# Kernel tuning notes

Measured on AMD Instinct MI355X. Metric: run time of the kernel, lower is better.

Reference implementation:

```python
import jax, jax.numpy as jnp
import numpy as np

NUM_FREQS = 10  # get_embedder_nerf(10, input_dims=3) -> 3 + 3*2*10 = 63 dims


def nerf_embed(x):
    # x: [..., 3]; order per NeRF embedder: [x, sin(f0*x), cos(f0*x), sin(f1*x), ...]
    freqs = (2.0 ** jnp.arange(NUM_FREQS)).astype(x.dtype)           # [10]
    xb = x[..., None, :] * freqs[:, None]                            # [..., 10, 3]
    sc = jnp.stack([jnp.sin(xb), jnp.cos(xb)], axis=-2)              # [..., 10, 2, 3]
    return jnp.concatenate([x, sc.reshape(x.shape[:-1] + (60,))], axis=-1)


def setup_inputs() -> dict:
    key = jax.random.key(0)
    ks = jax.random.split(key, 16)
    B, H, W = 4, 256, 256
    V, F = 50000, 100000
    FEAT, SHAPE_FEAT, STYLE = 256, 128, 256
    D_IN = FEAT + SHAPE_FEAT + 63 + STYLE  # 703
    HID = 256
    s = 0.05
    return {
        "pix_to_face": jax.random.randint(ks[0], (B, H, W), 0, F),
        "bary_coords": jax.random.uniform(ks[1], (B, H, W, 3), dtype=jnp.float32),
        "faces": jax.random.randint(ks[2], (F, 3), 0, V),
        "feature": jax.random.normal(ks[3], (V, FEAT), dtype=jnp.float32),
        "shape_features": jax.random.normal(ks[4], (V, SHAPE_FEAT), dtype=jnp.float32),
        "color_bg": jax.random.uniform(ks[5], (B, 3, 1, 1), dtype=jnp.float32),
        "style_latent": jax.random.normal(ks[6], (1, STYLE), dtype=jnp.float32),
        "w1": jax.random.normal(ks[7], (D_IN, HID), dtype=jnp.float32) * s,
        "b1": jax.random.normal(ks[8], (HID,), dtype=jnp.float32) * s,
        "w2": jax.random.normal(ks[9], (HID, HID), dtype=jnp.float32) * s,
        "b2": jax.random.normal(ks[10], (HID,), dtype=jnp.float32) * s,
        "w3": jax.random.normal(ks[11], (HID, 3), dtype=jnp.float32) * s,
        "b3": jax.random.normal(ks[12], (3,), dtype=jnp.float32) * s,
    }


def reference(pix_to_face, bary_coords, faces, feature, shape_features,
              color_bg, style_latent, w1, b1, w2, b2, w3, b3):
    B, H, W = pix_to_face.shape
    mask = pix_to_face > 0                                           # foreground pixels
    vidx = faces[pix_to_face]                                        # [B,H,W,3] vertex ids
    # gather per-vertex features then barycentric-weighted mean over the 3 verts
    fv = feature[vidx]                                               # [B,H,W,3,256]
    ff = jnp.einsum('bhwvc,bhwv->bhwc', fv, bary_coords) / 3.0       # .mean(dim=3)
    sv = shape_features[vidx]                                        # [B,H,W,3,128]
    sf = jnp.einsum('bhwvc,bhwv->bhwc', sv, bary_coords) / 3.0
    emb = nerf_embed(bary_coords)                                    # [B,H,W,63]
    style = jnp.broadcast_to(style_latent[0], (B, H, W, style_latent.shape[-1]))
    x = jnp.concatenate([ff, sf, emb, style], axis=-1)               # [B,H,W,703]
    h = jax.nn.relu(x @ w1 + b1)
    h = jax.nn.relu(h @ w2 + b2)
    out = jax.nn.relu(h @ w3 + b3)                                   # mlp ends with ReLU
    colors = out - 1.0                                               # use_act=True, tanh=False
    bg = color_bg[:, :, 0, 0][:, None, None, :]                      # [B,1,1,3]
    buf = jnp.where(mask[..., None], colors, bg)                     # scatter to image
    return jnp.concatenate([buf, mask.astype(buf.dtype)[..., None]], axis=-1)  # [B,H,W,4]
```

## Files before the change

### kernel.cpp

```cpp
#include <hip/hip_runtime.h>
#include <math.h>


typedef _Float16 hv8 __attribute__((ext_vector_type(8)));
typedef __attribute__((ext_vector_type(4))) float f32x4;

#define TILE_M 64

__device__ inline int swzE(int row, int k) { return row * 64  + (k ^ ((row & 7) << 3)); }
__device__ inline int swzH(int row, int k) { return row * 256 + (k ^ ((row & 7) << 3)); }
__device__ inline int swzA(int row, int k) { return row * 384 + (k ^ ((row & 7) << 3)); }

__global__ __launch_bounds__(256)
void prep_weights(const float* __restrict__ style,
                  const float* __restrict__ w1, const float* __restrict__ b1,
                  const float* __restrict__ w2, const float* __restrict__ w3,
                  _Float16* __restrict__ w1T, _Float16* __restrict__ w2T,
                  _Float16* __restrict__ w3T, float* __restrict__ b1p)
{
    const int j = blockIdx.x;
    const int t = threadIdx.x;
    if (j < 256) {
        float part = style[t] * w1[(size_t)(447 + t) * 256 + j];
        #pragma unroll
        for (int off = 32; off; off >>= 1) part += __shfl_down(part, off, 64);
        __shared__ float red[4];
        if ((t & 63) == 0) red[t >> 6] = part;
        __syncthreads();
        if (t == 0) b1p[j] = b1[j] + red[0] + red[1] + red[2] + red[3];
        for (int k = t; k < 448; k += 256) {
            float v = (k < 447) ? w1[(size_t)k * 256 + j] : 0.0f;
            if (k < 384) v *= (1.0f / 3.0f);
            w1T[(size_t)j * 448 + k] = (_Float16)v;
        }
    } else if (j < 512) {
        const int jj = j - 256;
        w2T[(size_t)jj * 256 + t] = (_Float16)w2[(size_t)t * 256 + jj];
    } else {
        #pragma unroll
        for (int r = 0; r < 16; ++r)
            w3T[r * 256 + t] = (r < 3) ? (_Float16)w3[t * 3 + r] : (_Float16)0.0f;
    }
}

__global__ __launch_bounds__(256, 2)
void pgemm(const float* __restrict__ feat, const float* __restrict__ shp,
           const _Float16* __restrict__ w1T, _Float16* __restrict__ P, int nV)
{
    __shared__ _Float16 as[64 * 384];
    const int tid = threadIdx.x;
    const int n0 = blockIdx.x * 64;
    const int lane = tid & 63, wv = tid >> 6;
    const int nbase = wv << 6, l15 = lane & 15, kq = lane >> 4;

    const hv8* bp[4];
    #pragma unroll
    for (int nf = 0; nf < 4; ++nf)
        bp[nf] = (const hv8*)(w1T + (size_t)(nbase + nf * 16 + l15) * 448 + (kq << 3));
    hv8 bv[3][4];
    auto loadB = [&](int t, hv8* dst) {
        #pragma unroll
        for (int nf = 0; nf < 4; ++nf) dst[nf] = bp[nf][t << 2];
    };
    loadB(0, bv[0]); loadB(1, bv[1]); loadB(2, bv[2]);

    #pragma unroll
    for (int i = 0; i < 12; ++i) {
        const int id = tid + i * 256;
        const int row = id / 48;
        const int g = id - row * 48;
        int v = n0 + row; if (v >= nV) v = nV - 1;
        const float* s = (g < 32) ? (feat + (size_t)v * 256 + g * 8)
                                  : (shp  + (size_t)v * 128 + (g - 32) * 8);
        const float4 a = ((const float4*)s)[0];
        const float4 b = ((const float4*)s)[1];
        hv8 h = { (_Float16)a.x, (_Float16)a.y, (_Float16)a.z, (_Float16)a.w,
                  (_Float16)b.x, (_Float16)b.y, (_Float16)b.z, (_Float16)b.w };
        *(hv8*)(&as[swzA(row, g * 8)]) = h;
    }
    f32x4 acc[4][4];
    #pragma unroll
    for (int mf = 0; mf < 4; ++mf)
        #pragma unroll
        for (int nf = 0; nf < 4; ++nf) acc[mf][nf] = (f32x4){0.f, 0.f, 0.f, 0.f};
    __syncthreads();

    auto loadA = [&](int t, hv8* dst) {
        #pragma unroll
        for (int mf = 0; mf < 4; ++mf)
            dst[mf] = *(const hv8*)(as + swzA(mf * 16 + l15, (t << 5) | (kq << 3)));
    };
    hv8 av[2][4];
    loadA(0, av[0]);
    #pragma unroll
    for (int t = 0; t < 12; ++t) {
        if (t + 1 < 12) loadA(t + 1, av[(t + 1) & 1]);
        const hv8* avt = av[t & 1];
        const hv8* bvt = bv[t % 3];
        __builtin_amdgcn_s_setprio(1);
        #pragma unroll
        for (int mf = 0; mf < 4; ++mf)
            #pragma unroll
            for (int nf = 0; nf < 4; ++nf)
                acc[mf][nf] = __builtin_amdgcn_mfma_f32_16x16x32_f16(avt[mf], bvt[nf], acc[mf][nf], 0, 0, 0);
        __builtin_amdgcn_s_setprio(0);
        if (t + 3 < 12) loadB(t + 3, bv[t % 3]);
    }
    #pragma unroll
    for (int mf = 0; mf < 4; ++mf)
        #pragma unroll
        for (int nf = 0; nf < 4; ++nf) {
            const int col = nbase + nf * 16 + l15;
            const int r0 = mf * 16 + (kq << 2);
            #pragma unroll
            for (int r = 0; r < 4; ++r) {
                const int v = n0 + r0 + r;
                if (v < nV) P[(size_t)v * 256 + col] = (_Float16)acc[mf][nf][r];
            }
        }
}

__global__ __launch_bounds__(512, 4)
void renderer(const int* __restrict__ pix, const float* __restrict__ bary,
              const int* __restrict__ faces,
              const _Float16* __restrict__ P,
              const float* __restrict__ color_bg,
              const float* __restrict__ b2g,
              const float* __restrict__ b3,
              const _Float16* __restrict__ w1T,
              const _Float16* __restrict__ w2T,
              const _Float16* __restrict__ w3T,
              const float* __restrict__ b1p,
              float* __restrict__ out)
{
    __shared__ _Float16 embs[64 * 64];
    __shared__ _Float16 pb[64 * 256];
    __shared__ int   vidx[TILE_M][3];
    __shared__ float bcs[TILE_M][3];

    const int tid = threadIdx.x;
    const int cpx = gridDim.x >> 3;
    const int bid = (blockIdx.x & 7) * cpx + (blockIdx.x >> 3);
    const int n0  = bid * TILE_M;

    const int lane  = tid & 63;
    const int wv    = tid >> 6;
    const int nbase = wv << 5;
    const int l15   = lane & 15;
    const int kq    = lane >> 4;

    if (tid < TILE_M) {
        const int n = n0 + tid;
        const int face = pix[n];
        vidx[tid][0] = faces[face * 3 + 0];
        vidx[tid][1] = faces[face * 3 + 1];
        vidx[tid][2] = faces[face * 3 + 2];
        bcs[tid][0] = bary[n * 3 + 0];
        bcs[tid][1] = bary[n * 3 + 1];
        bcs[tid][2] = bary[n * 3 + 2];
    }
    __syncthreads();

    const int gp = tid >> 5;
    const int c8 = (tid & 31) << 3;

    hv8 g0[3], g1[3];
    auto loadG = [&](hv8* g, const int b) {
        const int p = b * 16 + gp;
        g[0] = *(const hv8*)(P + (size_t)vidx[p][0] * 256 + c8);
        g[1] = *(const hv8*)(P + (size_t)vidx[p][1] * 256 + c8);
        g[2] = *(const hv8*)(P + (size_t)vidx[p][2] * 256 + c8);
    };
    auto blendG = [&](hv8* g, const int b) {
        const int p = b * 16 + gp;
        const _Float16 c0 = (_Float16)bcs[p][0];
        const _Float16 c1 = (_Float16)bcs[p][1];
        const _Float16 c2 = (_Float16)bcs[p][2];
        *(hv8*)(&pb[swzH(p, c8)]) = g[0] * c0 + g[1] * c1 + g[2] * c2;
    };

    loadG(g0, 0);
    loadG(g1, 1);

    {
        const int p = tid >> 3;
        const int e8 = (tid & 7) << 3;
        const float c0 = bcs[p][0], c1 = bcs[p][1], c2 = bcs[p][2];
        hv8 h;
        #pragma unroll
        for (int i = 0; i < 8; ++i) {
            const int s = e8 + i;
            float v;
            if (s < 3) v = (s == 0) ? c0 : ((s == 1) ? c1 : c2);
            else if (s < 63) {
                const int q = s - 3;
                const int f = q / 6;
                const int rem = q - f * 6;
                const int d = (rem >= 3) ? rem - 3 : rem;
                const float bd = (d == 0) ? c0 : ((d == 1) ? c1 : c2);
                const float arg = bd * (float)(1 << f);
                v = (rem < 3) ? __sinf(arg) : __cosf(arg);
            } else v = 0.0f;
            h[i] = (_Float16)v;
        }
        *(hv8*)(&embs[swzE(p, e8)]) = h;
    }

    blendG(g0, 0); loadG(g0, 2);
    blendG(g1, 1); loadG(g1, 3);
    blendG(g0, 2);
    blendG(g1, 3);

    f32x4 acc[4][2];
    #pragma unroll
    for (int nf = 0; nf < 2; ++nf) {
        const float b = b1p[nbase + nf * 16 + l15];
        #pragma unroll
        for (int mf = 0; mf < 4; ++mf) acc[mf][nf] = (f32x4){b, b, b, b};
    }
    __syncthreads();

    #pragma unroll
    for (int t = 0; t < 2; ++t) {
        hv8 ave[4], bve[2];
        #pragma unroll
        for (int nf = 0; nf < 2; ++nf)
            bve[nf] = *(const hv8*)(w1T + (size_t)(nbase + nf * 16 + l15) * 448 + 384 + (t << 5) + (kq << 3));
        #pragma unroll
        for (int mf = 0; mf < 4; ++mf)
            ave[mf] = *(const hv8*)(embs + swzE(mf * 16 + l15, (t << 5) | (kq << 3)));
        __builtin_amdgcn_s_setprio(1);
        #pragma unroll
        for (int mf = 0; mf < 4; ++mf)
            #pragma unroll
            for (int nf = 0; nf < 2; ++nf)
                acc[mf][nf] = __builtin_amdgcn_mfma_f32_16x16x32_f16(ave[mf], bve[nf], acc[mf][nf], 0, 0, 0);
        __builtin_amdgcn_s_setprio(0);
    }

    #pragma unroll
    for (int mf = 0; mf < 4; ++mf)
        #pragma unroll
        for (int nf = 0; nf < 2; ++nf) {
            const int col = nbase + nf * 16 + l15;
            const int r0 = mf * 16 + (kq << 2);
            #pragma unroll
            for (int r = 0; r < 4; ++r) {
                const int sl = swzH(r0 + r, col);
                const float pv = (float)pb[sl];
                pb[sl] = (_Float16)fmaxf(acc[mf][nf][r] + pv, 0.0f);
            }
            const float b = b2g[col];
            acc[mf][nf] = (f32x4){b, b, b, b};
        }
    __syncthreads();

    const hv8* bp2[2];
    #pragma unroll
    for (int nf = 0; nf < 2; ++nf)
        bp2[nf] = (const hv8*)(w2T + (size_t)(nbase + nf * 16 + l15) * 256 + (kq << 3));
    #pragma unroll
    for (int t = 0; t < 8; ++t) {
        hv8 av[4], bv[2];
        #pragma unroll
        for (int nf = 0; nf < 2; ++nf) bv[nf] = bp2[nf][t << 2];
        #pragma unroll
        for (int mf = 0; mf < 4; ++mf)
            av[mf] = *(const hv8*)(pb + swzH(mf * 16 + l15, (t << 5) | (kq << 3)));
        __builtin_amdgcn_s_setprio(1);
        #pragma unroll
        for (int mf = 0; mf < 4; ++mf)
            #pragma unroll
            for (int nf = 0; nf < 2; ++nf)
                acc[mf][nf] = __builtin_amdgcn_mfma_f32_16x16x32_f16(av[mf], bv[nf], acc[mf][nf], 0, 0, 0);
        __builtin_amdgcn_s_setprio(0);
    }

    __syncthreads();
    #pragma unroll
    for (int mf = 0; mf < 4; ++mf)
        #pragma unroll
        for (int nf = 0; nf < 2; ++nf) {
            const int col = nbase + nf * 16 + l15;
            const int r0 = mf * 16 + (kq << 2);
            #pragma unroll
            for (int r = 0; r < 4; ++r)
                pb[swzH(r0 + r, col)] = (_Float16)fmaxf(acc[mf][nf][r], 0.0f);
        }

    hv8 bw3[8];
    if (wv < 4) {
        #pragma unroll
        for (int t = 0; t < 8; ++t)
            bw3[t] = *(const hv8*)(w3T + l15 * 256 + ((t << 5) | (kq << 3)));
    }
    __syncthreads();

    if (wv < 4) {
        f32x4 acc3 = (f32x4){0.f, 0.f, 0.f, 0.f};
        #pragma unroll
        for (int t = 0; t < 8; ++t) {
            const hv8 av3 = *(const hv8*)(pb + swzH((wv << 4) + l15, (t << 5) | (kq << 3)));
            acc3 = __builtin_amdgcn_mfma_f32_16x16x32_f16(av3, bw3[t], acc3, 0, 0, 0);
        }
        if (l15 < 4) {
            const int ch = l15;
            #pragma unroll
            for (int r = 0; r < 4; ++r) {
                const int p = (wv << 4) + (kq << 2) + r;
                const int n = n0 + p;
                const bool m = pix[n] > 0;
                float v;
                if (ch == 3) v = m ? 1.0f : 0.0f;
                else         v = m ? (fmaxf(acc3[r] + b3[ch], 0.0f) - 1.0f)
                                   : color_bg[(n >> 16) * 3 + ch];
                out[(size_t)n * 4 + ch] = v;
            }
        }
    }
}

extern "C" void kernel_launch(void* const* d_in, const int* in_sizes, int n_in,
                              void* d_out, int out_size, void* d_ws, size_t ws_size,
                              hipStream_t stream) {
    const int*   pix      = (const int*)  d_in[0];
    const float* bary     = (const float*)d_in[1];
    const int*   faces    = (const int*)  d_in[2];
    const float* feature  = (const float*)d_in[3];
    const float* shapef   = (const float*)d_in[4];
    const float* color_bg = (const float*)d_in[5];
    const float* style    = (const float*)d_in[6];
    const float* w1       = (const float*)d_in[7];
    const float* b1       = (const float*)d_in[8];
    const float* w2       = (const float*)d_in[9];
    const float* b2       = (const float*)d_in[10];
    const float* w3       = (const float*)d_in[11];
    const float* b3       = (const float*)d_in[12];
    float* out = (float*)d_out;

    const int nV = in_sizes[3] / 256;

    char* ws = (char*)d_ws;
    _Float16* w1T  = (_Float16*)ws;
    _Float16* w2T  = (_Float16*)(ws + 229376);
    float*    b1p  = (float*)   (ws + 360448);
    _Float16* w3T  = (_Float16*)(ws + 361472);
    _Float16* Ptab = (_Float16*)(ws + 369664);

    hipLaunchKernelGGL(prep_weights, dim3(513), dim3(256), 0, stream,
                       style, w1, b1, w2, w3, w1T, w2T, w3T, b1p);
    hipLaunchKernelGGL(pgemm, dim3((nV + 63) / 64), dim3(256), 0, stream,
                       feature, shapef, w1T, Ptab, nV);

    const int npix = in_sizes[0];
    hipLaunchKernelGGL(renderer, dim3(npix / TILE_M), dim3(512), 0, stream,
                       pix, bary, faces, Ptab, color_bg,
                       b2, b3, w1T, w2T, w3T, b1p, out);
}
```

Baseline: 183.3 us.

## Process two pixel tiles per block, overlapping next tile's gathers with layer-2 MFMAs

The renderer block now handles 128 pixels as two 64-pixel sub-tiles with double-buffered shared activation tiles and metadata. The vertex-feature gathers, barycentric blend and embedding computation for the second sub-tile are interleaved with the layer-2 MFMA loop of the first, hiding gather latency behind matrix work. The cost is doubled shared memory (about 74KB per block), which may reduce occupancy, and the grid is halved.

```diff
diff --git a/kernel.cpp b/kernel.cpp
--- a/kernel.cpp
+++ b/kernel.cpp
@@ -4,8 +4,6 @@
 
 typedef _Float16 hv8 __attribute__((ext_vector_type(8)));
 typedef __attribute__((ext_vector_type(4))) float f32x4;
-
-#define TILE_M 64
 
 __device__ inline int swzE(int row, int k) { return row * 64  + (k ^ ((row & 7) << 3)); }
 __device__ inline int swzH(int row, int k) { return row * 256 + (k ^ ((row & 7) << 3)); }
@@ -126,74 +124,69 @@
               const _Float16* __restrict__ P,
               const float* __restrict__ color_bg,
               const float* __restrict__ b2g,
-              const float* __restrict__ b3,
+              const float* __restrict__ b3g,
               const _Float16* __restrict__ w1T,
               const _Float16* __restrict__ w2T,
               const _Float16* __restrict__ w3T,
               const float* __restrict__ b1p,
               float* __restrict__ out)
 {
+    __shared__ _Float16 pb[2][64 * 256];
     __shared__ _Float16 embs[64 * 64];
-    __shared__ _Float16 pb[64 * 256];
-    __shared__ int   vidx[TILE_M][3];
-    __shared__ float bcs[TILE_M][3];
+    __shared__ int   vidx[2][64][3];
+    __shared__ float bcs[2][64][3];
 
     const int tid = threadIdx.x;
     const int cpx = gridDim.x >> 3;
     const int bid = (blockIdx.x & 7) * cpx + (blockIdx.x >> 3);
-    const int n0  = bid * TILE_M;
+    const int nb  = bid * 128;
 
     const int lane  = tid & 63;
     const int wv    = tid >> 6;
     const int nbase = wv << 5;
     const int l15   = lane & 15;
     const int kq    = lane >> 4;
-
-    if (tid < TILE_M) {
-        const int n = n0 + tid;
-        const int face = pix[n];
-        vidx[tid][0] = faces[face * 3 + 0];
-        vidx[tid][1] = faces[face * 3 + 1];
-        vidx[tid][2] = faces[face * 3 + 2];
-        bcs[tid][0] = bary[n * 3 + 0];
-        bcs[tid][1] = bary[n * 3 + 1];
-        bcs[tid][2] = bary[n * 3 + 2];
-    }
-    __syncthreads();
-
-    const int gp = tid >> 5;
-    const int c8 = (tid & 31) << 3;
-
+    const int gp    = tid >> 5;
+    const int c8    = (tid & 31) << 3;
+
+    auto metaLoad = [&](int s) {
+        if (tid < 64) {
+            const int n = nb + (s << 6) + tid;
+            const int face = pix[n];
+            vidx[s][tid][0] = faces[face * 3 + 0];
+            vidx[s][tid][1] = faces[face * 3 + 1];
+            vidx[s][tid][2] = faces[face * 3 + 2];
+            bcs[s][tid][0] = bary[n * 3 + 0];
+            bcs[s][tid][1] = bary[n * 3 + 1];
+            bcs[s][tid][2] = bary[n * 3 + 2];
+        }
+    };
     hv8 g0[3], g1[3];
-    auto loadG = [&](hv8* g, const int b) {
-        const int p = b * 16 + gp;
-        g[0] = *(const hv8*)(P + (size_t)vidx[p][0] * 256 + c8);
-        g[1] = *(const hv8*)(P + (size_t)vidx[p][1] * 256 + c8);
-        g[2] = *(const hv8*)(P + (size_t)vidx[p][2] * 256 + c8);
-    };
-    auto blendG = [&](hv8* g, const int b) {
-        const int p = b * 16 + gp;
-        const _Float16 c0 = (_Float16)bcs[p][0];
-        const _Float16 c1 = (_Float16)bcs[p][1];
-        const _Float16 c2 = (_Float16)bcs[p][2];
-        *(hv8*)(&pb[swzH(p, c8)]) = g[0] * c0 + g[1] * c1 + g[2] * c2;
-    };
-
-    loadG(g0, 0);
-    loadG(g1, 1);
-
-    {
+    auto loadG = [&](hv8* g, int s, int b) {
+        const int p = (b << 4) + gp;
+        g[0] = *(const hv8*)(P + (size_t)vidx[s][p][0] * 256 + c8);
+        g[1] = *(const hv8*)(P + (size_t)vidx[s][p][1] * 256 + c8);
+        g[2] = *(const hv8*)(P + (size_t)vidx[s][p][2] * 256 + c8);
+    };
+    auto blendG = [&](hv8* g, int s, int b) {
+        const int p = (b << 4) + gp;
+        const _Float16 d0 = (_Float16)bcs[s][p][0];
+        const _Float16 d1 = (_Float16)bcs[s][p][1];
+        const _Float16 d2 = (_Float16)bcs[s][p][2];
+        *(hv8*)(&pb[s][swzH(p, c8)]) = g[0] * d0 + g[1] * d1 + g[2] * d2;
+    };
+    auto embPhase = [&](int s) {
         const int p = tid >> 3;
         const int e8 = (tid & 7) << 3;
-        const float c0 = bcs[p][0], c1 = bcs[p][1], c2 = bcs[p][2];
+        const float c0 = bcs[s][p][0], c1 = bcs[s][p][1], c2 = bcs[s][p][2];
         hv8 h;
         #pragma unroll
         for (int i = 0; i < 8; ++i) {
-            const int s = e8 + i;
+            const int sl = e8 + i;
             float v;
-            if (s < 3) v = (s == 0) ? c0 : ((s == 1) ? c1 : c2);
-            else if (s < 63) {
-                const int q = s - 3;
+            if (sl < 3) v = (sl == 0) ? c0 : ((sl == 1) ? c1 : c2);
+            else if (sl < 63) {
+                const int q = sl - 3;
                 const int f = q / 6;
                 const int rem = q - f * 6;
                 const int d = (rem >= 3) ? rem - 3 : rem;
@@ -204,69 +197,64 @@
             h[i] = (_Float16)v;
         }
         *(hv8*)(&embs[swzE(p, e8)]) = h;
-    }
-
-    blendG(g0, 0); loadG(g0, 2);
-    blendG(g1, 1); loadG(g1, 3);
-    blendG(g0, 2);
-    blendG(g1, 3);
+    };
 
     f32x4 acc[4][2];
-    #pragma unroll
-    for (int nf = 0; nf < 2; ++nf) {
-        const float b = b1p[nbase + nf * 16 + l15];
-        #pragma unroll
-        for (int mf = 0; mf < 4; ++mf) acc[mf][nf] = (f32x4){b, b, b, b};
-    }
-    __syncthreads();
-
-    #pragma unroll
-    for (int t = 0; t < 2; ++t) {
-        hv8 ave[4], bve[2];
-        #pragma unroll
-        for (int nf = 0; nf < 2; ++nf)
-            bve[nf] = *(const hv8*)(w1T + (size_t)(nbase + nf * 16 + l15) * 448 + 384 + (t << 5) + (kq << 3));
-        #pragma unroll
-        for (int mf = 0; mf < 4; ++mf)
-            ave[mf] = *(const hv8*)(embs + swzE(mf * 16 + l15, (t << 5) | (kq << 3)));
-        __builtin_amdgcn_s_setprio(1);
-        #pragma unroll
-        for (int mf = 0; mf < 4; ++mf)
+    auto accB1 = [&]() {
+        #pragma unroll
+        for (int nf = 0; nf < 2; ++nf) {
+            const float b = b1p[nbase + nf * 16 + l15];
+            #pragma unroll
+            for (int mf = 0; mf < 4; ++mf) acc[mf][nf] = (f32x4){b, b, b, b};
+        }
+    };
+    auto l1mfma = [&]() {
+        #pragma unroll
+        for (int t = 0; t < 2; ++t) {
+            hv8 ave[4], bve[2];
             #pragma unroll
             for (int nf = 0; nf < 2; ++nf)
-                acc[mf][nf] = __builtin_amdgcn_mfma_f32_16x16x32_f16(ave[mf], bve[nf], acc[mf][nf], 0, 0, 0);
-        __builtin_amdgcn_s_setprio(0);
-    }
-
-    #pragma unroll
-    for (int mf = 0; mf < 4; ++mf)
-        #pragma unroll
-        for (int nf = 0; nf < 2; ++nf) {
-            const int col = nbase + nf * 16 + l15;
-            const int r0 = mf * 16 + (kq << 2);
-            #pragma unroll
-            for (int r = 0; r < 4; ++r) {
-                const int sl = swzH(r0 + r, col);
-                const float pv = (float)pb[sl];
-                pb[sl] = (_Float16)fmaxf(acc[mf][nf][r] + pv, 0.0f);
-            }
-            const float b = b2g[col];
-            acc[mf][nf] = (f32x4){b, b, b, b};
-        }
-    __syncthreads();
-
+                bve[nf] = *(const hv8*)(w1T + (size_t)(nbase + nf * 16 + l15) * 448 + 384 + (t << 5) + (kq << 3));
+            #pragma unroll
+            for (int mf = 0; mf < 4; ++mf)
+                ave[mf] = *(const hv8*)(embs + swzE(mf * 16 + l15, (t << 5) | (kq << 3)));
+            __builtin_amdgcn_s_setprio(1);
+            #pragma unroll
+            for (int mf = 0; mf < 4; ++mf)
+                #pragma unroll
+                for (int nf = 0; nf < 2; ++nf)
+                    acc[mf][nf] = __builtin_amdgcn_mfma_f32_16x16x32_f16(ave[mf], bve[nf], acc[mf][nf], 0, 0, 0);
+            __builtin_amdgcn_s_setprio(0);
+        }
+    };
+    auto l1epi = [&](int s) {
+        #pragma unroll
+        for (int mf = 0; mf < 4; ++mf)
+            #pragma unroll
+            for (int nf = 0; nf < 2; ++nf) {
+                const int col = nbase + nf * 16 + l15;
+                const int r0 = mf * 16 + (kq << 2);
+                #pragma unroll
+                for (int r = 0; r < 4; ++r) {
+                    const int sl = swzH(r0 + r, col);
+                    const float pv = (float)pb[s][sl];
+                    pb[s][sl] = (_Float16)fmaxf(acc[mf][nf][r] + pv, 0.0f);
+                }
+                const float b = b2g[col];
+                acc[mf][nf] = (f32x4){b, b, b, b};
+            }
+    };
     const hv8* bp2[2];
     #pragma unroll
     for (int nf = 0; nf < 2; ++nf)
         bp2[nf] = (const hv8*)(w2T + (size_t)(nbase + nf * 16 + l15) * 256 + (kq << 3));
-    #pragma unroll
-    for (int t = 0; t < 8; ++t) {
+    auto l2tile = [&](int s, int t) {
         hv8 av[4], bv[2];
         #pragma unroll
         for (int nf = 0; nf < 2; ++nf) bv[nf] = bp2[nf][t << 2];
         #pragma unroll
         for (int mf = 0; mf < 4; ++mf)
-            av[mf] = *(const hv8*)(pb + swzH(mf * 16 + l15, (t << 5) | (kq << 3)));
+            av[mf] = *(const hv8*)(pb[s] + swzH(mf * 16 + l15, (t << 5) | (kq << 3)));
         __builtin_amdgcn_s_setprio(1);
         #pragma unroll
         for (int mf = 0; mf < 4; ++mf)
@@ -274,50 +262,89 @@
             for (int nf = 0; nf < 2; ++nf)
                 acc[mf][nf] = __builtin_amdgcn_mfma_f32_16x16x32_f16(av[mf], bv[nf], acc[mf][nf], 0, 0, 0);
         __builtin_amdgcn_s_setprio(0);
-    }
-
-    __syncthreads();
-    #pragma unroll
-    for (int mf = 0; mf < 4; ++mf)
-        #pragma unroll
-        for (int nf = 0; nf < 2; ++nf) {
-            const int col = nbase + nf * 16 + l15;
-            const int r0 = mf * 16 + (kq << 2);
-            #pragma unroll
-            for (int r = 0; r < 4; ++r)
-                pb[swzH(r0 + r, col)] = (_Float16)fmaxf(acc[mf][nf][r], 0.0f);
-        }
-
-    hv8 bw3[8];
-    if (wv < 4) {
-        #pragma unroll
-        for (int t = 0; t < 8; ++t)
-            bw3[t] = *(const hv8*)(w3T + l15 * 256 + ((t << 5) | (kq << 3)));
-    }
-    __syncthreads();
-
-    if (wv < 4) {
-        f32x4 acc3 = (f32x4){0.f, 0.f, 0.f, 0.f};
-        #pragma unroll
-        for (int t = 0; t < 8; ++t) {
-            const hv8 av3 = *(const hv8*)(pb + swzH((wv << 4) + l15, (t << 5) | (kq << 3)));
-            acc3 = __builtin_amdgcn_mfma_f32_16x16x32_f16(av3, bw3[t], acc3, 0, 0, 0);
-        }
-        if (l15 < 4) {
-            const int ch = l15;
-            #pragma unroll
-            for (int r = 0; r < 4; ++r) {
-                const int p = (wv << 4) + (kq << 2) + r;
-                const int n = n0 + p;
-                const bool m = pix[n] > 0;
-                float v;
-                if (ch == 3) v = m ? 1.0f : 0.0f;
-                else         v = m ? (fmaxf(acc3[r] + b3[ch], 0.0f) - 1.0f)
-                                   : color_bg[(n >> 16) * 3 + ch];
-                out[(size_t)n * 4 + ch] = v;
-            }
-        }
-    }
+    };
+    auto h2wr = [&](int s) {
+        #pragma unroll
+        for (int mf = 0; mf < 4; ++mf)
+            #pragma unroll
+            for (int nf = 0; nf < 2; ++nf) {
+                const int col = nbase + nf * 16 + l15;
+                const int r0 = mf * 16 + (kq << 2);
+                #pragma unroll
+                for (int r = 0; r < 4; ++r)
+                    pb[s][swzH(r0 + r, col)] = (_Float16)fmaxf(acc[mf][nf][r], 0.0f);
+            }
+    };
+    auto l3out = [&](int s) {
+        if (wv < 4) {
+            hv8 bw3[8];
+            #pragma unroll
+            for (int t = 0; t < 8; ++t)
+                bw3[t] = *(const hv8*)(w3T + l15 * 256 + (t << 5) + (kq << 3));
+            f32x4 acc3 = (f32x4){0.f, 0.f, 0.f, 0.f};
+            #pragma unroll
+            for (int t = 0; t < 8; ++t) {
+                const hv8 a3 = *(const hv8*)(pb[s] + swzH((wv << 4) + l15, (t << 5) | (kq << 3)));
+                acc3 = __builtin_amdgcn_mfma_f32_16x16x32_f16(a3, bw3[t], acc3, 0, 0, 0);
+            }
+            if (l15 < 4) {
+                const int ch = l15;
+                #pragma unroll
+                for (int r = 0; r < 4; ++r) {
+                    const int p = (wv << 4) + (kq << 2) + r;
+                    const int n = nb + (s << 6) + p;
+                    const bool m = pix[n] > 0;
+                    float v;
+                    if (ch == 3) v = m ? 1.0f : 0.0f;
+                    else         v = m ? (fmaxf(acc3[r] + b3g[ch], 0.0f) - 1.0f)
+                                       : color_bg[(n >> 16) * 3 + ch];
+                    out[(size_t)n * 4 + ch] = v;
+                }
+            }
+        }
+    };
+
+    metaLoad(0);
+    __syncthreads();
+
+    loadG(g0, 0, 0); loadG(g1, 0, 1);
+    embPhase(0);
+    blendG(g0, 0, 0); loadG(g0, 0, 2);
+    blendG(g1, 0, 1); loadG(g1, 0, 3);
+    blendG(g0, 0, 2);
+    blendG(g1, 0, 3);
+    accB1();
+    __syncthreads();
+
+    l1mfma();
+    l1epi(0);
+    metaLoad(1);
+    __syncthreads();
+
+    l2tile(0, 0); loadG(g0, 1, 0);
+    l2tile(0, 1); blendG(g0, 1, 0); loadG(g1, 1, 1);
+    l2tile(0, 2); blendG(g1, 1, 1); loadG(g0, 1, 2);
+    l2tile(0, 3); blendG(g0, 1, 2); loadG(g1, 1, 3);
+    l2tile(0, 4); blendG(g1, 1, 3);
+    l2tile(0, 5); embPhase(1);
+    l2tile(0, 6);
+    l2tile(0, 7);
+    __syncthreads();
+
+    h2wr(0);
+    accB1();
+    __syncthreads();
+    l3out(0);
+
+    l1mfma();
+    l1epi(1);
+    __syncthreads();
+    l2tile(1, 0); l2tile(1, 1); l2tile(1, 2); l2tile(1, 3);
+    l2tile(1, 4); l2tile(1, 5); l2tile(1, 6); l2tile(1, 7);
+    __syncthreads();
+    h2wr(1);
+    __syncthreads();
+    l3out(1);
 }
 
 extern "C" void kernel_launch(void* const* d_in, const int* in_sizes, int n_in,
@@ -353,7 +380,7 @@
                        feature, shapef, w1T, Ptab, nV);
 
     const int npix = in_sizes[0];
-    hipLaunchKernelGGL(renderer, dim3(npix / TILE_M), dim3(512), 0, stream,
+    hipLaunchKernelGGL(renderer, dim3(npix / 128), dim3(512), 0, stream,
                        pix, bary, faces, Ptab, color_bg,
                        b2, b3, w1T, w2T, w3T, b1p, out);
 }
```

Result: slower. 215.9 us (+17.7%).
